# Kernel tuning notes

Hardware: AMD Instinct MI355X
Metric: run time of the kernel (lower is better)

## Reference

```python
import jax, jax.numpy as jnp
import numpy as np

N, H, DK, DV, DFF, D = 2, 8, 32, 32, 512, 256
B, S = 2, 2048
MASK_VALUE = -1e-30
EPS = 1e-14  # K.epsilon()**2 with default epsilon 1e-7


def glorot(key, shape):
    fan_in, fan_out = shape[-2], shape[-1]
    limit = np.sqrt(6.0 / (fan_in + fan_out))
    return jax.random.uniform(key, shape, jnp.float32, -limit, limit)


def setup_inputs() -> dict:
    key = jax.random.key(0)
    ks = jax.random.split(key, 8)
    return {
        "x": jax.random.normal(ks[0], (B, S, D), jnp.float32),
        "mask": jnp.ones((B, S), jnp.float32),
        "Wq": glorot(ks[1], (N, H, D, DK)),
        "Wk": glorot(ks[2], (N, H, D, DK)),
        "Wv": glorot(ks[3], (N, H, D, DV)),
        "Wo": glorot(ks[4], (N, H * DV, D)),
        "W1": glorot(ks[5], (N, D, DFF)),
        "b1": jnp.zeros((N, DFF), jnp.float32),
        "W2": glorot(ks[6], (N, DFF, D)),
        "b2": jnp.zeros((N, D), jnp.float32),
        "gamma": jnp.ones((2 * N,), jnp.float32),
        "beta": jnp.zeros((2 * N,), jnp.float32),
    }


def _layernorm(x, g, b):
    mean = jnp.mean(x, axis=-1, keepdims=True)
    var = jnp.mean(jnp.square(x - mean), axis=-1, keepdims=True)
    return (x - mean) / jnp.sqrt(var + EPS) * g + b


def reference(x, mask, Wq, Wk, Wv, Wo, W1, b1, W2, b2, gamma, beta):
    m = mask[:, None, None, :]  # [B,1,1,S], multiplies score rows' key axis
    for i in range(N):
        # batched multi-head attention (no 1/sqrt(dk) scaling, faithful to source)
        q = jnp.einsum("bsd,hdk->bhsk", x, Wq[i])
        k = jnp.einsum("bsd,hdk->bhsk", x, Wk[i])
        v = jnp.einsum("bsd,hdv->bhsv", x, Wv[i])
        A = jnp.einsum("bhsk,bhtk->bhst", q, k)  # [B,H,S,S]
        A = m * A + (1.0 - m) * MASK_VALUE
        A = jax.nn.softmax(A, axis=-1)
        o = jnp.einsum("bhst,bhtv->bhsv", A, v)
        conc = o.transpose(0, 2, 1, 3).reshape(x.shape[0], x.shape[1], H * DV)
        x = x + conc @ Wo[i]
        x = _layernorm(x, gamma[2 * i], beta[2 * i])
        ffn = jax.nn.relu(x @ W1[i] + b1[i]) @ W2[i] + b2[i]
        x = x + ffn
        x = _layernorm(x, gamma[2 * i + 1], beta[2 * i + 1])
    return x
```

## Files before the change

### kernel.cpp

```cpp
#include <hip/hip_runtime.h>
#include <hip/hip_bf16.h>

#define NL 2
#define NH 8
#define DKk 32
#define DVv 32
#define DFF 512
#define DD 256
#define BB 2
#define SS 2048
#define MROWS (BB*SS)
#define LN_EPS 1e-14f
#define L2E 1.4426950408889634f
#define SOFT_SHIFT_L2E (50.0f*L2E)

typedef __hip_bfloat16 bf16;
typedef unsigned short us;
typedef short bf16x8 __attribute__((ext_vector_type(8)));
typedef float f32x4  __attribute__((ext_vector_type(4)));
typedef unsigned short us4 __attribute__((ext_vector_type(4)));

#define O_XF   256
#define O_QB   (O_XF+1048576)
#define O_KH   (O_QB+1048576)
#define O_KL   (O_KH+524288)
#define O_VT   (O_KL+524288)
#define O_XH   (O_VT+524288)
#define O_XL   (O_XH+524288)
#define O_OP   (O_XL+524288)
#define O_ML   (O_OP+2097152)
#define O_MASK (O_ML+65536)
#define O_B1   (O_MASK+4096)
#define O_B2   (O_B1+1024)
#define O_GM   (O_B2+512)
#define O_BT   (O_GM+4)
#define O_PREP (O_BT+4)
#define CONV_TOTAL (1048576+4096+1024+512+4+4)
#define CONV_BLOCKS ((CONV_TOTAL+255)/256)
#define PREP_BLOCKS 512
#define PQH 0u
#define PQL 393216u
#define POH 786432u
#define POL 917504u
#define P1H 1048576u
#define P1L 1310720u
#define P2H 1572864u
#define P2L 1835008u

__device__ __forceinline__ float us2f(us u){
  unsigned int v = ((unsigned int)u) << 16; float f;
  __builtin_memcpy(&f, &v, 4); return f;
}
__device__ __forceinline__ us f2bf_rne(float f){
  unsigned int b = __float_as_uint(f);
  b += 0x7FFFu + ((b>>16)&1u);
  return (us)(b>>16);
}

#if __has_builtin(__builtin_amdgcn_exp2f)
#define EXP2F(x) __builtin_amdgcn_exp2f(x)
#else
#define EXP2F(x) exp2f(x)
#endif

#if __has_builtin(__builtin_amdgcn_cvt_pk_bf16_f32)
typedef __bf16 bf16x2_t __attribute__((ext_vector_type(2)));
__device__ __forceinline__ int pack_bf16(float a, float b){
  bf16x2_t r = __builtin_amdgcn_cvt_pk_bf16_f32(a, b);
  int i; __builtin_memcpy(&i, &r, 4); return i;
}
#else
__device__ __forceinline__ int pack_bf16(float a, float b){
  int b0 = __float_as_int(a) + 0x8000;
  int b1 = __float_as_int(b) + 0x8000;
  return (b1 & 0xFFFF0000) | ((int)((unsigned)b0 >> 16));
}
#endif

__device__ __forceinline__ void gl_lds16(const us* g, us* l){
  __builtin_amdgcn_global_load_lds(
    (const __attribute__((address_space(1))) unsigned int*)g,
    (__attribute__((address_space(3))) unsigned int*)l, 16, 0, 0);
}

__device__ __forceinline__ size_t xhl_idx(int row, int col){
  int rt = row>>6, rg = (row>>4)&3, L15 = row&15;
  int kc = col>>5, Q = (col>>3)&3, j = col&7;
  return ((size_t)(rt*8+kc))*2048 + rg*512 + Q*128 + L15*8 + j;
}

__device__ __forceinline__ float conv1(const void* src, size_t i, int flag){
  if(flag) return ((const float*)src)[i];
  return us2f(((const us*)src)[i]);
}

__device__ __forceinline__ void prep_b_raw(const void* W0, const void* W1v, const void* W2v,
                                           int baseoff, us* __restrict__ Bh, us* __restrict__ Bl,
                                           int Kd, int Nd, int qkv, int g, int flag)
{
  int total = (Kd/32)*(Nd/16)*64;
  if(g >= total) return;
  int lane = g & 63, fi = g >> 6;
  int ncN = Nd/16;
  int nc = fi % ncN, kc = fi / ncN;
  int Q = lane>>4, L15 = lane&15;
  int n = nc*16 + L15;
  const void* src;
  int off0, stride;
  if(qkv){
    int sec = n>>8, h = (n>>5)&7, kq = n&31;
    src = (sec==0)?W0:((sec==1)?W1v:W2v);
    off0 = baseoff + h*8192 + kq;
    stride = 32;
  } else {
    src = W0;
    off0 = baseoff + n;
    stride = Nd;
  }
  #pragma unroll
  for(int j=0;j<8;j++){
    int k = kc*32 + Q*8 + j;
    float v = conv1(src, (size_t)off0 + (size_t)k*stride, flag);
    us hb = f2bf_rne(v);
    Bh[(size_t)g*8 + j] = hb;
    Bl[(size_t)g*8 + j] = f2bf_rne(v - us2f(hb));
  }
}

__global__ void conv_prep(const void* s0, const void* s1, const void* sWq, const void* sWk,
                          const void* sWv, const void* sWo, const void* sW1, const void* sb1,
                          const void* sW2, const void* sb2, const void* sgm, const void* sbt,
                          float* __restrict__ ws, int* __restrict__ flagp)
{
  __shared__ int fsh[4];
  int bad = 0;
  const us* xr = (const us*)s0;
  for(int i=threadIdx.x; i<4096; i+=256){
    float f = us2f(xr[i]);
    if(!(fabsf(f) < 1e3f)) bad = 1;
  }
  unsigned long long m = __ballot(bad);
  if((threadIdx.x&63)==0) fsh[threadIdx.x>>6] = (m!=0ull);
  __syncthreads();
  int flag = (fsh[0]|fsh[1]|fsh[2]|fsh[3]);
  if(blockIdx.x==0 && threadIdx.x==0) *flagp = flag;

  int b = blockIdx.x;
  if(b < PREP_BLOCKS){
    int layer = b >> 8, lb = b & 255;
    us* prep = (us*)(ws + O_PREP);
    if(lb < 96){
      int g = lb*256 + threadIdx.x;
      prep_b_raw(sWq, sWk, sWv, layer*65536, prep+PQH+(size_t)layer*196608,
                 prep+PQL+(size_t)layer*196608, 256, 768, 1, g, flag);
    } else if(lb < 128){
      int g = (lb-96)*256 + threadIdx.x;
      prep_b_raw(sWo, nullptr, nullptr, layer*65536, prep+POH+(size_t)layer*65536,
                 prep+POL+(size_t)layer*65536, 256, 256, 0, g, flag);
    } else if(lb < 192){
      int g = (lb-128)*256 + threadIdx.x;
      prep_b_raw(sW1, nullptr, nullptr, layer*131072, prep+P1H+(size_t)layer*131072,
                 prep+P1L+(size_t)layer*131072, 256, 512, 0, g, flag);
    } else {
      int g = (lb-192)*256 + threadIdx.x;
      prep_b_raw(sW2, nullptr, nullptr, layer*131072, prep+P2H+(size_t)layer*131072,
                 prep+P2L+(size_t)layer*131072, 512, 256, 0, g, flag);
    }
    return;
  }
  int g = (b - PREP_BLOCKS)*256 + threadIdx.x;
  if(g < 1048576){
    float v = conv1(s0, g, flag);
    ws[O_XF+g] = v;
    us hb = f2bf_rne(v);
    us lb = f2bf_rne(v - us2f(hb));
    size_t xi = xhl_idx(g>>8, g&255);
    ((us*)(ws+O_XH))[xi] = hb;
    ((us*)(ws+O_XL))[xi] = lb;
    return;
  }
  g -= 1048576;
  if(g < 4096){ ws[O_MASK+g] = conv1(s1, g, flag)*L2E; return; }
  g -= 4096;
  if(g < 1024){ ws[O_B1+g] = conv1(sb1, g, flag); return; }
  g -= 1024;
  if(g < 512){ ws[O_B2+g] = conv1(sb2, g, flag); return; }
  g -= 512;
  if(g < 4){ ws[O_GM+g] = conv1(sgm, g, flag); return; }
  g -= 4;
  if(g < 4){ ws[O_BT+g] = conv1(sbt, g, flag); return; }
}

template<int MODE>
__launch_bounds__(256)
__global__ void gemm_mfma(const us* __restrict__ Axh, const us* __restrict__ Axl,
                          const us* __restrict__ Bh, const us* __restrict__ Bl,
                          const float* __restrict__ bias,
                          float* __restrict__ O,
                          us* __restrict__ QH, us* __restrict__ QL,
                          us* __restrict__ KH, us* __restrict__ KL, us* __restrict__ VT,
                          int Ncols, int Kdim)
{
  __shared__ __align__(16) us SH[16384];
  const int t = threadIdx.x;
  const int w = t>>6, lane = t&63;
  const int Q = lane>>4, L15 = lane&15;
  const int bx = blockIdx.x, by = blockIdx.y;
  const int row0 = bx*64;
  const int nc0 = by*4;
  const int col0 = by*64;
  const int nKc = Kdim>>5;
  const int ncW = Ncols>>4;

  f32x4 acc[2][2];
  #pragma unroll
  for(int i=0;i<2;i++)
    #pragma unroll
    for(int j=0;j<2;j++) acc[i][j] = (f32x4){0.f,0.f,0.f,0.f};

  auto stage = [&](int kc){
    const int bo = (kc&1)*8192;
    size_t abase = ((size_t)(bx*nKc + kc))*2048;
    gl_lds16(&Axh[abase + (size_t)t*8], &SH[bo + t*8]);
    gl_lds16(&Axl[abase + (size_t)t*8], &SH[bo + 2048 + t*8]);
    size_t gidx = ((size_t)(kc*ncW + nc0 + w)*64 + lane)*8;
    gl_lds16(&Bh[gidx], &SH[bo + 4096 + t*8]);
    gl_lds16(&Bl[gidx], &SH[bo + 6144 + t*8]);
  };

  stage(0);

  for(int kc=0; kc<nKc; kc++){
    __syncthreads();
    if(kc+1 < nKc) stage(kc+1);
    const int bo = (kc&1)*8192;
    const us* Ah  = SH + bo;
    const us* Al  = SH + bo + 2048;
    const us* Bhs = SH + bo + 4096;
    const us* Bls = SH + bo + 6144;

    bf16x8 aAh[2], aAl[2], bBh[2], bBl[2];
    #pragma unroll
    for(int rg2=0;rg2<2;rg2++){
      int rg = (w&1)*2 + rg2;
      aAh[rg2] = *(const bf16x8*)&Ah[rg*512 + lane*8];
      aAl[rg2] = *(const bf16x8*)&Al[rg*512 + lane*8];
    }
    #pragma unroll
    for(int cg2=0;cg2<2;cg2++){
      int nc = (w>>1)*2 + cg2;
      bBh[cg2] = *(const bf16x8*)&Bhs[nc*512 + lane*8];
      bBl[cg2] = *(const bf16x8*)&Bls[nc*512 + lane*8];
    }
    #pragma unroll
    for(int rg2=0;rg2<2;rg2++)
      #pragma unroll
      for(int cg2=0;cg2<2;cg2++){
        acc[rg2][cg2] = __builtin_amdgcn_mfma_f32_16x16x32_bf16(aAl[rg2], bBh[cg2], acc[rg2][cg2], 0,0,0);
        acc[rg2][cg2] = __builtin_amdgcn_mfma_f32_16x16x32_bf16(aAh[rg2], bBl[cg2], acc[rg2][cg2], 0,0,0);
        acc[rg2][cg2] = __builtin_amdgcn_mfma_f32_16x16x32_bf16(aAh[rg2], bBh[cg2], acc[rg2][cg2], 0,0,0);
      }
  }

  if(MODE==0){
    __syncthreads();
    us* TH = SH;
    us* TL = SH + 4608;
    #pragma unroll
    for(int rg2=0;rg2<2;rg2++)
      #pragma unroll
      for(int cg2=0;cg2<2;cg2++)
        #pragma unroll
        for(int r=0;r<4;r++){
          int rl = (w&1)*32 + rg2*16 + Q*4 + r;
          int cl = (w>>1)*32 + cg2*16 + L15;
          float va = acc[rg2][cg2][r];
          us hb = f2bf_rne(va);
          TH[rl*72+cl] = hb;
          TL[rl*72+cl] = f2bf_rne(va - us2f(hb));
        }
    __syncthreads();
    const int sec = col0>>8;
    const int h0  = (col0&255)>>5;
    const int b_  = row0>>11;
    const int srow0 = row0 & 2047;
    if(sec < 2){
      us* DH = (sec==0) ? QH : KH;
      us* DL = (sec==0) ? QL : KL;
      #pragma unroll
      for(int u2=0; u2<2; u2++){
        int u = w + u2*4;
        int rg = u&3, half = u>>2;
        int lbase = (rg*16 + L15)*72 + half*32 + Q*8;
        bf16x8 hv = *(const bf16x8*)&TH[lbase];
        bf16x8 lv = *(const bf16x8*)&TL[lbase];
        int bh = b_*NH + h0 + half;
        size_t dbase = ((size_t)(bh*128 + (srow0>>4) + rg)*64 + lane)*8;
        *(bf16x8*)&DH[dbase] = hv;
        *(bf16x8*)&DL[dbase] = lv;
      }
    } else {
      #pragma unroll
      for(int u2=0; u2<2; u2++){
        int u = w + u2*4;
        int sgrp = u&1, kqh = (u>>1)&1, half = u>>2;
        union{ us u8[8]; bf16x8 v; } vv;
        #pragma unroll
        for(int j=0;j<8;j++){
          int rl = sgrp*32 + Q*8 + j;
          int cl = half*32 + kqh*16 + L15;
          vv.u8[j] = TH[rl*72+cl];
        }
        int bh = b_*NH + h0 + half;
        size_t dbase = ((size_t)((bh*64 + (srow0>>5) + sgrp)*2 + kqh)*64 + lane)*8;
        *(bf16x8*)&VT[dbase] = vv.v;
      }
    }
  } else {
    #pragma unroll
    for(int rg2=0;rg2<2;rg2++)
      #pragma unroll
      for(int cg2=0;cg2<2;cg2++)
        #pragma unroll
        for(int r=0;r<4;r++){
          int row = row0 + (w&1)*32 + rg2*16 + Q*4 + r;
          int c   = col0 + (w>>1)*32 + cg2*16 + L15;
          float v = acc[rg2][cg2][r] + bias[c];
          O[(size_t)row*Ncols + c] = v>0.f ? v : 0.f;
        }
  }
}

template<int SRC>
__launch_bounds__(256)
__global__ void gemm_ln(const float* __restrict__ A,
                        const float* __restrict__ OpartA, const float* __restrict__ MLA,
                        const us* __restrict__ Bh, const us* __restrict__ Bl,
                        const float* __restrict__ bias, const float* __restrict__ res,
                        float* __restrict__ xf,
                        us* __restrict__ xh, us* __restrict__ xl,
                        const float* __restrict__ gamma, const float* __restrict__ beta, int gi,
                        void* __restrict__ out, int write_out,
                        const int* __restrict__ flagp, int Kdim)
{
  __shared__ __align__(16) us Ahs[1024], Als[1024];
  __shared__ __align__(16) us Bhs[16384], Bls[16384];
  __shared__ float lred[128];
  const int t = threadIdx.x;
  const int w = t>>6, lane = t&63;
  const int Q = lane>>4, L15 = lane&15;
  const int row0 = blockIdx.x*16;
  const int nKc = Kdim>>5;

  f32x4 acc[4];
  #pragma unroll
  for(int cg=0;cg<4;cg++) acc[cg] = (f32x4){0.f,0.f,0.f,0.f};

  float4 pv0, pv1, pv;
  float pl0 = 0.f, pl1 = 0.f;

  auto preloadA = [&](int kc){
    if(t < 128){
      int r = t>>3;
      int kl = (t&7)*4;
      if(SRC==0){
        int row = row0 + r;
        int b_ = row>>11, s_ = row&2047;
        size_t i0 = (size_t)(b_*8 + kc)*2048 + s_;
        pl0 = MLA[i0];
        pl1 = MLA[i0+32768];
        pv0 = *(const float4*)&OpartA[i0*32 + kl];
        pv1 = *(const float4*)&OpartA[(i0+32768)*32 + kl];
      } else {
        pv = *(const float4*)&A[(size_t)(row0+r)*Kdim + kc*32 + kl];
      }
    }
  };
  auto writeA = [&](int kc){
    if(t < 128){
      int r = t>>3;
      int kl = (t&7)*4;
      float f[4];
      if(SRC==0){
        float inv = 1.f/(pl0 + pl1);
        f[0]=(pv0.x+pv1.x)*inv; f[1]=(pv0.y+pv1.y)*inv;
        f[2]=(pv0.z+pv1.z)*inv; f[3]=(pv0.w+pv1.w)*inv;
      } else {
        f[0]=pv.x; f[1]=pv.y; f[2]=pv.z; f[3]=pv.w;
      }
      us4 h4, l4;
      #pragma unroll
      for(int j=0;j<4;j++){
        us hb = f2bf_rne(f[j]);
        h4[j] = hb; l4[j] = f2bf_rne(f[j] - us2f(hb));
      }
      int bo = (kc&1)*512;
      int off = (kl>>3)*128 + r*8 + (kl&7);
      *(us4*)&Ahs[bo+off] = h4;
      *(us4*)&Als[bo+off] = l4;
    }
  };
  auto stageB = [&](int kc){
    const int bo = (kc&1)*8192;
    #pragma unroll
    for(int ii=0; ii<4; ii++){
      int unit = w + ii*4;
      size_t gidx = ((size_t)(kc*16 + unit)*64 + lane)*8;
      gl_lds16(&Bh[gidx], &Bhs[bo + unit*512 + lane*8]);
      gl_lds16(&Bl[gidx], &Bls[bo + unit*512 + lane*8]);
    }
  };

  preloadA(0);
  stageB(0);
  writeA(0);

  for(int kc=0; kc<nKc; kc++){
    __syncthreads();
    if(kc+1 < nKc){
      preloadA(kc+1);
      stageB(kc+1);
    }
    const int bo = (kc&1);
    bf16x8 aAh = *(const bf16x8*)&Ahs[bo*512 + lane*8];
    bf16x8 aAl = *(const bf16x8*)&Als[bo*512 + lane*8];
    #pragma unroll
    for(int cg=0;cg<4;cg++){
      int unit = w*4 + cg;
      bf16x8 bBh = *(const bf16x8*)&Bhs[bo*8192 + unit*512 + lane*8];
      bf16x8 bBl = *(const bf16x8*)&Bls[bo*8192 + unit*512 + lane*8];
      acc[cg] = __builtin_amdgcn_mfma_f32_16x16x32_bf16(aAl, bBh, acc[cg], 0,0,0);
      acc[cg] = __builtin_amdgcn_mfma_f32_16x16x32_bf16(aAh, bBl, acc[cg], 0,0,0);
      acc[cg] = __builtin_amdgcn_mfma_f32_16x16x32_bf16(aAh, bBh, acc[cg], 0,0,0);
    }
    if(kc+1 < nKc) writeA(kc+1);
  }

  float tmp[4][4];
  #pragma unroll
  for(int cg=0;cg<4;cg++)
    #pragma unroll
    for(int r=0;r<4;r++){
      int row = row0 + Q*4 + r;
      int c = w*64 + cg*16 + L15;
      float v = acc[cg][r] + res[(size_t)row*DD + c];
      if(SRC==1) v += bias[c];
      tmp[cg][r] = v;
    }
  float s[4], sq[4];
  #pragma unroll
  for(int r=0;r<4;r++){
    s[r]  = tmp[0][r]+tmp[1][r]+tmp[2][r]+tmp[3][r];
    sq[r] = tmp[0][r]*tmp[0][r]+tmp[1][r]*tmp[1][r]+tmp[2][r]*tmp[2][r]+tmp[3][r]*tmp[3][r];
  }
  #pragma unroll
  for(int off=1; off<16; off<<=1)
    #pragma unroll
    for(int r=0;r<4;r++){
      s[r]  += __shfl_xor(s[r], off);
      sq[r] += __shfl_xor(sq[r], off);
    }
  if(L15==0){
    #pragma unroll
    for(int r=0;r<4;r++){
      int rl = Q*4 + r;
      lred[(w*16 + rl)*2]   = s[r];
      lred[(w*16 + rl)*2+1] = sq[r];
    }
  }
  __syncthreads();
  float g = gamma[gi], bb = beta[gi];
  float scv[4], mnv[4];
  #pragma unroll
  for(int r=0;r<4;r++){
    int rl = Q*4 + r;
    float S  = lred[rl*2]   + lred[(16+rl)*2]   + lred[(32+rl)*2]   + lred[(48+rl)*2];
    float SQ = lred[rl*2+1] + lred[(16+rl)*2+1] + lred[(32+rl)*2+1] + lred[(48+rl)*2+1];
    float mean = S*(1.f/DD);
    float var  = SQ*(1.f/DD) - mean*mean;
    scv[r] = rsqrtf(var+LN_EPS)*g;
    mnv[r] = mean;
  }
  int flag = write_out ? *flagp : 0;
  #pragma unroll
  for(int cg=0;cg<4;cg++)
    #pragma unroll
    for(int r=0;r<4;r++){
      int row = row0 + Q*4 + r;
      int c = w*64 + cg*16 + L15;
      float val = (tmp[cg][r]-mnv[r])*scv[r] + bb;
      xf[(size_t)row*DD + c] = val;
      us hb = f2bf_rne(val);
      size_t xi = xhl_idx(row, c);
      xh[xi] = hb;
      xl[xi] = f2bf_rne(val - us2f(hb));
      if(write_out){
        if(flag) ((float*)out)[(size_t)row*DD + c] = val;
        else     ((bf16*)out)[(size_t)row*DD + c] = __float2bfloat16(val);
      }
    }
}

__launch_bounds__(256)
__global__ void attn_kernel(const us* __restrict__ QH, const us* __restrict__ QL,
                            const us* __restrict__ KH, const us* __restrict__ KL,
                            const us* __restrict__ VT,
                            const float* __restrict__ mask,
                            float* __restrict__ Opart, float* __restrict__ ML)
{
  __shared__ __align__(16) us Khs[4096], Kls[4096], Vts[4096];
  __shared__ __align__(16) float Msl[128];
  const int t = threadIdx.x;
  const int bh = blockIdx.x >> 6;
  const int qt = (blockIdx.x & 63) >> 1;
  const int ks = blockIdx.x & 1;
  const int b_ = bh >> 3;
  const int wv = t >> 6;
  const int lane = t & 63;
  const int Q = lane >> 4, L15 = lane & 15;
  const int q0 = qt*64 + wv*16;

  size_t qidx = ((size_t)(bh*128 + qt*4 + wv)*64 + lane)*8;
  const bf16x8 qh_v = *(const bf16x8*)&QH[qidx];
  const bf16x8 ql_v = *(const bf16x8*)&QL[qidx];

  const us* KHbh = KH + (size_t)bh*65536;
  const us* KLbh = KL + (size_t)bh*65536;
  const us* VTbh = VT + (size_t)bh*65536;
  const int base = ks*1024;

  f32x4 Oa0a = {0.f,0.f,0.f,0.f}, Oa0b = {0.f,0.f,0.f,0.f};
  f32x4 Oa1a = {0.f,0.f,0.f,0.f}, Oa1b = {0.f,0.f,0.f,0.f};
  float lacc = 0.f;

  {
    size_t kbase = (size_t)(base>>4)*512;
    size_t vbase = (size_t)(base>>5)*1024;
    gl_lds16(&KHbh[kbase + (size_t)t*8], &Khs[t*8]);
    gl_lds16(&KLbh[kbase + (size_t)t*8], &Kls[t*8]);
    gl_lds16(&VTbh[vbase + (size_t)t*8], &Vts[t*8]);
    if(t < 64) Msl[t] = mask[b_*SS + base + t];
  }

  for(int s=0; s<16; s++){
    __syncthreads();
    if(s < 15){
      int t0n = base + (s+1)*64;
      int bn = (s+1)&1;
      size_t kbase = (size_t)(t0n>>4)*512;
      size_t vbase = (size_t)(t0n>>5)*1024;
      gl_lds16(&KHbh[kbase + (size_t)t*8], &Khs[bn*2048 + t*8]);
      gl_lds16(&KLbh[kbase + (size_t)t*8], &Kls[bn*2048 + t*8]);
      gl_lds16(&VTbh[vbase + (size_t)t*8], &Vts[bn*2048 + t*8]);
      if(t < 64) Msl[bn*64 + t] = mask[b_*SS + t0n + t];
    }
    const int bo = (s&1)*2048;
    const int mo = (s&1)*64;

    f32x4 St[4];
    const f32x4 zz = {0.f,0.f,0.f,0.f};
    #pragma unroll
    for(int kt=0;kt<4;kt++){
      bf16x8 aKh = *(const bf16x8*)&Khs[bo + kt*512 + lane*8];
      bf16x8 aKl = *(const bf16x8*)&Kls[bo + kt*512 + lane*8];
      f32x4 a = __builtin_amdgcn_mfma_f32_16x16x32_bf16(aKl, qh_v, zz, 0,0,0);
      a = __builtin_amdgcn_mfma_f32_16x16x32_bf16(aKh, ql_v, a, 0,0,0);
      a = __builtin_amdgcn_mfma_f32_16x16x32_bf16(aKh, qh_v, a, 0,0,0);
      St[kt] = a;
    }

    float lsum = 0.f;
    #pragma unroll
    for(int kt=0;kt<4;kt++){
      float4 mv = *(const float4*)&Msl[mo + kt*16 + Q*4];
      float mvr[4] = {mv.x, mv.y, mv.z, mv.w};
      #pragma unroll
      for(int r=0;r<4;r++){
        float p = EXP2F(fmaf(mvr[r], St[kt][r], -SOFT_SHIFT_L2E));
        St[kt][r] = p;
        lsum += p;
      }
    }
    lacc += lsum;

    int pk[4][2];
    #pragma unroll
    for(int kt=0;kt<4;kt++){
      pk[kt][0] = pack_bf16(St[kt][0], St[kt][1]);
      pk[kt][1] = pack_bf16(St[kt][2], St[kt][3]);
    }

    #pragma unroll
    for(int c=0;c<2;c++){
      union { int i[4]; bf16x8 v; } bu;
      #pragma unroll
      for(int d=0;d<4;d++){
        int srcl = (((Q&1)*2 + (d>>1))<<4) | L15;
        int vlo = __shfl(pk[2*c  ][d&1], srcl, 64);
        int vhi = __shfl(pk[2*c+1][d&1], srcl, 64);
        bu.i[d] = (Q & 2) ? vhi : vlo;
      }
      bf16x8 aV0 = *(const bf16x8*)&Vts[bo + (c*2+0)*512 + lane*8];
      bf16x8 aV1 = *(const bf16x8*)&Vts[bo + (c*2+1)*512 + lane*8];
      if(c == 0){
        Oa0a = __builtin_amdgcn_mfma_f32_16x16x32_bf16(aV0, bu.v, Oa0a, 0,0,0);
        Oa1a = __builtin_amdgcn_mfma_f32_16x16x32_bf16(aV1, bu.v, Oa1a, 0,0,0);
      } else {
        Oa0b = __builtin_amdgcn_mfma_f32_16x16x32_bf16(aV0, bu.v, Oa0b, 0,0,0);
        Oa1b = __builtin_amdgcn_mfma_f32_16x16x32_bf16(aV1, bu.v, Oa1b, 0,0,0);
      }
    }
  }

  f32x4 Oa0 = Oa0a + Oa0b;
  f32x4 Oa1 = Oa1a + Oa1b;
  lacc += __shfl_xor(lacc, 16);
  lacc += __shfl_xor(lacc, 32);

  float* opp = &Opart[((size_t)(ks*16+bh)*SS + q0 + L15)*32];
  #pragma unroll
  for(int r=0;r<4;r++){
    opp[Q*4+r]    = Oa0[r];
    opp[16+Q*4+r] = Oa1[r];
  }
  if(Q==0){
    ML[(size_t)(ks*16+bh)*SS + q0 + L15] = lacc;
  }
}

extern "C" void kernel_launch(void* const* d_in, const int* in_sizes, int n_in,
                              void* d_out, int out_size, void* d_ws, size_t ws_size,
                              hipStream_t stream)
{
  float* ws = (float*)d_ws;
  int* flagp = (int*)d_ws;

  float* xf  = ws + O_XF;
  us* QHb = (us*)(ws + O_QB);
  us* QLb = QHb + 1048576;
  us* KH = (us*)(ws + O_KH);
  us* KL = (us*)(ws + O_KL);
  us* VT = (us*)(ws + O_VT);
  us* XH = (us*)(ws + O_XH);
  us* XL = (us*)(ws + O_XL);
  float* Opart = ws + O_OP;
  float* ML  = ws + O_ML;
  float* fh  = Opart;
  float* b1f = ws + O_B1;
  float* b2f_ = ws + O_B2;
  float* gmf = ws + O_GM;
  float* btf = ws + O_BT;
  us* prep = (us*)(ws + O_PREP);

  conv_prep<<<PREP_BLOCKS+CONV_BLOCKS,256,0,stream>>>(
      d_in[0], d_in[1], d_in[2], d_in[3], d_in[4], d_in[5],
      d_in[6], d_in[7], d_in[8], d_in[9], d_in[10], d_in[11],
      ws, flagp);

  for(int i=0;i<NL;i++){
    const float* b1i = b1f + (size_t)i*DFF;
    const float* b2i = b2f_ + (size_t)i*DD;

    dim3 g0(64, 12);
    gemm_mfma<0><<<g0,256,0,stream>>>(XH, XL,
                                      prep+PQH+(size_t)i*196608, prep+PQL+(size_t)i*196608,
                                      nullptr, nullptr,
                                      QHb, QLb, KH, KL, VT, 768, 256);
    attn_kernel<<<1024,256,0,stream>>>(QHb, QLb, KH, KL, VT, ws + O_MASK, Opart, ML);
    gemm_ln<0><<<256,256,0,stream>>>(nullptr, Opart, ML,
                                     prep+POH+(size_t)i*65536, prep+POL+(size_t)i*65536,
                                     nullptr, xf, xf, XH, XL,
                                     gmf, btf, 2*i, d_out, 0, flagp, 256);
    dim3 g2(64, 8);
    gemm_mfma<2><<<g2,256,0,stream>>>(XH, XL,
                                      prep+P1H+(size_t)i*131072, prep+P1L+(size_t)i*131072,
                                      b1i, fh,
                                      nullptr, nullptr, nullptr, nullptr, nullptr, 512, 256);
    gemm_ln<1><<<256,256,0,stream>>>(fh, nullptr, nullptr,
                                     prep+P2H+(size_t)i*131072, prep+P2L+(size_t)i*131072,
                                     b2i, xf, xf, XH, XL,
                                     gmf, btf, 2*i+1, d_out, (i==NL-1)?1:0, flagp, 512);
  }
}
```

Measured before the change: 258.7 us.

## Triple-buffer LDS staging with explicit vmcnt waits in GEMM and attention kernels

Switches the async global-to-LDS staging in the MFMA GEMM, GEMM+LayerNorm and attention kernels from double to triple buffering, prefetching two chunks ahead. The full __syncthreads is replaced with a partial s_waitcnt vmcnt plus a raw barrier, so later loads can stay in flight while the current chunk is computed. The attention kernel also loads the whole 1024-entry mask slice into LDS once up front instead of per step. This hides more global load latency, at the cost of more LDS per block, which may reduce occupancy, and it depends on hand-counted vmcnt values being correct.

```diff
diff --git a/kernel.cpp b/kernel.cpp
--- a/kernel.cpp
+++ b/kernel.cpp
@@ -47,6 +47,11 @@
 #define P2H 1572864u
 #define P2L 1835008u
 
+#define WAITVMC(n) asm volatile("s_waitcnt vmcnt(" #n ")" ::: "memory")
+#define LGKM0()    asm volatile("s_waitcnt lgkmcnt(0)" ::: "memory")
+#define SBAR()     __builtin_amdgcn_s_barrier()
+#define SCHEDB()   __builtin_amdgcn_sched_barrier(0)
+
 __device__ __forceinline__ float us2f(us u){
   unsigned int v = ((unsigned int)u) << 16; float f;
   __builtin_memcpy(&f, &v, 4); return f;
@@ -201,7 +206,7 @@
                           us* __restrict__ KH, us* __restrict__ KL, us* __restrict__ VT,
                           int Ncols, int Kdim)
 {
-  __shared__ __align__(16) us SH[16384];
+  __shared__ __align__(16) us SH[24576];
   const int t = threadIdx.x;
   const int w = t>>6, lane = t&63;
   const int Q = lane>>4, L15 = lane&15;
@@ -218,8 +223,8 @@
     #pragma unroll
     for(int j=0;j<2;j++) acc[i][j] = (f32x4){0.f,0.f,0.f,0.f};
 
-  auto stage = [&](int kc){
-    const int bo = (kc&1)*8192;
+  auto stage = [&](int kc, int bi){
+    const int bo = bi*8192;
     size_t abase = ((size_t)(bx*nKc + kc))*2048;
     gl_lds16(&Axh[abase + (size_t)t*8], &SH[bo + t*8]);
     gl_lds16(&Axl[abase + (size_t)t*8], &SH[bo + 2048 + t*8]);
@@ -228,12 +233,18 @@
     gl_lds16(&Bl[gidx], &SH[bo + 6144 + t*8]);
   };
 
-  stage(0);
-
+  stage(0, 0);
+  stage(1, 1);
+
+  int rb = 0;
   for(int kc=0; kc<nKc; kc++){
-    __syncthreads();
-    if(kc+1 < nKc) stage(kc+1);
-    const int bo = (kc&1)*8192;
+    if(kc+1 < nKc){ WAITVMC(4); } else { WAITVMC(0); }
+    SCHEDB();
+    SBAR();
+    SCHEDB();
+    if(kc+2 < nKc) stage(kc+2, rb==0 ? 2 : rb-1);
+
+    const int bo = rb*8192;
     const us* Ah  = SH + bo;
     const us* Al  = SH + bo + 2048;
     const us* Bhs = SH + bo + 4096;
@@ -260,6 +271,7 @@
         acc[rg2][cg2] = __builtin_amdgcn_mfma_f32_16x16x32_bf16(aAh[rg2], bBl[cg2], acc[rg2][cg2], 0,0,0);
         acc[rg2][cg2] = __builtin_amdgcn_mfma_f32_16x16x32_bf16(aAh[rg2], bBh[cg2], acc[rg2][cg2], 0,0,0);
       }
+    rb = rb==2 ? 0 : rb+1;
   }
 
   if(MODE==0){
@@ -344,7 +356,7 @@
                         const int* __restrict__ flagp, int Kdim)
 {
   __shared__ __align__(16) us Ahs[1024], Als[1024];
-  __shared__ __align__(16) us Bhs[16384], Bls[16384];
+  __shared__ __align__(16) us Bhs[24576], Bls[24576];
   __shared__ float lred[128];
   const int t = threadIdx.x;
   const int w = t>>6, lane = t&63;
@@ -400,8 +412,8 @@
       *(us4*)&Als[bo+off] = l4;
     }
   };
-  auto stageB = [&](int kc){
-    const int bo = (kc&1)*8192;
+  auto stageB = [&](int kc, int bi){
+    const int bo = bi*8192;
     #pragma unroll
     for(int ii=0; ii<4; ii++){
       int unit = w + ii*4;
@@ -412,28 +424,34 @@
   };
 
   preloadA(0);
-  stageB(0);
+  stageB(0, 0);
+  stageB(1, 1);
   writeA(0);
 
+  int rb = 0;
   for(int kc=0; kc<nKc; kc++){
-    __syncthreads();
-    if(kc+1 < nKc){
-      preloadA(kc+1);
-      stageB(kc+1);
-    }
-    const int bo = (kc&1);
-    bf16x8 aAh = *(const bf16x8*)&Ahs[bo*512 + lane*8];
-    bf16x8 aAl = *(const bf16x8*)&Als[bo*512 + lane*8];
+    if(kc+1 < nKc){ WAITVMC(8); } else { WAITVMC(0); }
+    LGKM0();
+    SCHEDB();
+    SBAR();
+    SCHEDB();
+    if(kc+1 < nKc) preloadA(kc+1);
+    if(kc+2 < nKc) stageB(kc+2, rb==0 ? 2 : rb-1);
+
+    const int bo = rb*8192;
+    bf16x8 aAh = *(const bf16x8*)&Ahs[(kc&1)*512 + lane*8];
+    bf16x8 aAl = *(const bf16x8*)&Als[(kc&1)*512 + lane*8];
     #pragma unroll
     for(int cg=0;cg<4;cg++){
       int unit = w*4 + cg;
-      bf16x8 bBh = *(const bf16x8*)&Bhs[bo*8192 + unit*512 + lane*8];
-      bf16x8 bBl = *(const bf16x8*)&Bls[bo*8192 + unit*512 + lane*8];
+      bf16x8 bBh = *(const bf16x8*)&Bhs[bo + unit*512 + lane*8];
+      bf16x8 bBl = *(const bf16x8*)&Bls[bo + unit*512 + lane*8];
       acc[cg] = __builtin_amdgcn_mfma_f32_16x16x32_bf16(aAl, bBh, acc[cg], 0,0,0);
       acc[cg] = __builtin_amdgcn_mfma_f32_16x16x32_bf16(aAh, bBl, acc[cg], 0,0,0);
       acc[cg] = __builtin_amdgcn_mfma_f32_16x16x32_bf16(aAh, bBh, acc[cg], 0,0,0);
     }
     if(kc+1 < nKc) writeA(kc+1);
+    rb = rb==2 ? 0 : rb+1;
   }
 
   float tmp[4][4];
@@ -508,8 +526,8 @@
                             const float* __restrict__ mask,
                             float* __restrict__ Opart, float* __restrict__ ML)
 {
-  __shared__ __align__(16) us Khs[4096], Kls[4096], Vts[4096];
-  __shared__ __align__(16) float Msl[128];
+  __shared__ __align__(16) us Khs[6144], Kls[6144], Vts[6144];
+  __shared__ __align__(16) float Msl[1024];
   const int t = threadIdx.x;
   const int bh = blockIdx.x >> 6;
   const int qt = (blockIdx.x & 63) >> 1;
@@ -533,29 +551,32 @@
   f32x4 Oa1a = {0.f,0.f,0.f,0.f}, Oa1b = {0.f,0.f,0.f,0.f};
   float lacc = 0.f;
 
+  auto stagekv = [&](int s, int bi){
+    int t0n = base + s*64;
+    size_t kbase = (size_t)(t0n>>4)*512;
+    size_t vbase = (size_t)(t0n>>5)*1024;
+    gl_lds16(&KHbh[kbase + (size_t)t*8], &Khs[bi*2048 + t*8]);
+    gl_lds16(&KLbh[kbase + (size_t)t*8], &Kls[bi*2048 + t*8]);
+    gl_lds16(&VTbh[vbase + (size_t)t*8], &Vts[bi*2048 + t*8]);
+  };
+
   {
-    size_t kbase = (size_t)(base>>4)*512;
-    size_t vbase = (size_t)(base>>5)*1024;
-    gl_lds16(&KHbh[kbase + (size_t)t*8], &Khs[t*8]);
-    gl_lds16(&KLbh[kbase + (size_t)t*8], &Kls[t*8]);
-    gl_lds16(&VTbh[vbase + (size_t)t*8], &Vts[t*8]);
-    if(t < 64) Msl[t] = mask[b_*SS + base + t];
-  }
-
+    const us* mrow = (const us*)(mask + (size_t)b_*SS + base);
+    gl_lds16(mrow + (size_t)t*8, ((us*)Msl) + t*8);
+    stagekv(0, 0);
+    stagekv(1, 1);
+  }
+
+  int rb = 0;
   for(int s=0; s<16; s++){
-    __syncthreads();
-    if(s < 15){
-      int t0n = base + (s+1)*64;
-      int bn = (s+1)&1;
-      size_t kbase = (size_t)(t0n>>4)*512;
-      size_t vbase = (size_t)(t0n>>5)*1024;
-      gl_lds16(&KHbh[kbase + (size_t)t*8], &Khs[bn*2048 + t*8]);
-      gl_lds16(&KLbh[kbase + (size_t)t*8], &Kls[bn*2048 + t*8]);
-      gl_lds16(&VTbh[vbase + (size_t)t*8], &Vts[bn*2048 + t*8]);
-      if(t < 64) Msl[bn*64 + t] = mask[b_*SS + t0n + t];
-    }
-    const int bo = (s&1)*2048;
-    const int mo = (s&1)*64;
+    if(s+1 < 16){ WAITVMC(3); } else { WAITVMC(0); }
+    SCHEDB();
+    SBAR();
+    SCHEDB();
+    if(s+2 < 16) stagekv(s+2, rb==0 ? 2 : rb-1);
+
+    const int bo = rb*2048;
+    const int mo = s*64;
 
     f32x4 St[4];
     const f32x4 zz = {0.f,0.f,0.f,0.f};
@@ -610,6 +631,7 @@
         Oa1b = __builtin_amdgcn_mfma_f32_16x16x32_bf16(aV1, bu.v, Oa1b, 0,0,0);
       }
     }
+    rb = rb==2 ? 0 : rb+1;
   }
 
   f32x4 Oa0 = Oa0a + Oa0b;
```

New measurement: 274.9 us. 1.06x slower.

## Vectorize input conversion, swizzle attention block order, preload full mask slice

Applied to the files above, without the earlier changes.

The input conversion now handles 8 elements per thread with 16-byte loads and stores for the float, hi and lo copies, replacing scalar per-element writes. The attention kernel remaps block indices so neighbouring workgroups are spread across head/query tiles, which is meant to improve cache locality or the spread of work across XCDs. It also loads the whole 1024-entry mask slice into LDS once with an async copy instead of per-iteration scalar loads. The cost is more LDS use and a fixed 8-way swizzle that assumes the grid size is 1024 blocks.

```diff
diff --git a/kernel.cpp b/kernel.cpp
--- a/kernel.cpp
+++ b/kernel.cpp
@@ -35,8 +35,8 @@
 #define O_GM   (O_B2+512)
 #define O_BT   (O_GM+4)
 #define O_PREP (O_BT+4)
-#define CONV_TOTAL (1048576+4096+1024+512+4+4)
-#define CONV_BLOCKS ((CONV_TOTAL+255)/256)
+#define TAIL_TOTAL (4096+1024+512+4+4)
+#define CONV_BLOCKS (512 + (TAIL_TOTAL+255)/256)
 #define PREP_BLOCKS 512
 #define PQH 0u
 #define PQL 393216u
@@ -168,18 +168,36 @@
     }
     return;
   }
-  int g = (b - PREP_BLOCKS)*256 + threadIdx.x;
-  if(g < 1048576){
-    float v = conv1(s0, g, flag);
-    ws[O_XF+g] = v;
-    us hb = f2bf_rne(v);
-    us lb = f2bf_rne(v - us2f(hb));
-    size_t xi = xhl_idx(g>>8, g&255);
-    ((us*)(ws+O_XH))[xi] = hb;
-    ((us*)(ws+O_XL))[xi] = lb;
+  int b2 = b - PREP_BLOCKS;
+  if(b2 < 512){
+    int g8 = b2*256 + threadIdx.x;
+    int e0 = g8*8;
+    float v[8];
+    if(flag){
+      float4 a0 = *((const float4*)s0 + (e0>>2));
+      float4 a1 = *((const float4*)s0 + (e0>>2) + 1);
+      v[0]=a0.x; v[1]=a0.y; v[2]=a0.z; v[3]=a0.w;
+      v[4]=a1.x; v[5]=a1.y; v[6]=a1.z; v[7]=a1.w;
+    } else {
+      bf16x8 u = *((const bf16x8*)s0 + g8);
+      #pragma unroll
+      for(int j=0;j<8;j++) v[j] = us2f((us)u[j]);
+    }
+    *(float4*)&ws[O_XF+e0]   = (float4){v[0],v[1],v[2],v[3]};
+    *(float4*)&ws[O_XF+e0+4] = (float4){v[4],v[5],v[6],v[7]};
+    union{ us a[8]; uint4 q; } hh, ll;
+    #pragma unroll
+    for(int j=0;j<8;j++){
+      us hb = f2bf_rne(v[j]);
+      hh.a[j] = hb;
+      ll.a[j] = f2bf_rne(v[j] - us2f(hb));
+    }
+    size_t xi = xhl_idx(e0>>8, e0&255);
+    *(uint4*)&((us*)(ws+O_XH))[xi] = hh.q;
+    *(uint4*)&((us*)(ws+O_XL))[xi] = ll.q;
     return;
   }
-  g -= 1048576;
+  int g = (b2-512)*256 + threadIdx.x;
   if(g < 4096){ ws[O_MASK+g] = conv1(s1, g, flag)*L2E; return; }
   g -= 4096;
   if(g < 1024){ ws[O_B1+g] = conv1(sb1, g, flag); return; }
@@ -509,11 +527,12 @@
                             float* __restrict__ Opart, float* __restrict__ ML)
 {
   __shared__ __align__(16) us Khs[4096], Kls[4096], Vts[4096];
-  __shared__ __align__(16) float Msl[128];
+  __shared__ __align__(16) float Msl[1024];
   const int t = threadIdx.x;
-  const int bh = blockIdx.x >> 6;
-  const int qt = (blockIdx.x & 63) >> 1;
-  const int ks = blockIdx.x & 1;
+  const int swz = (blockIdx.x & 7)*128 + (blockIdx.x >> 3);
+  const int bh = swz >> 6;
+  const int qt = (swz & 63) >> 1;
+  const int ks = swz & 1;
   const int b_ = bh >> 3;
   const int wv = t >> 6;
   const int lane = t & 63;
@@ -534,12 +553,13 @@
   float lacc = 0.f;
 
   {
+    const us* mrow = (const us*)(mask + (size_t)b_*SS + base);
+    gl_lds16(mrow + (size_t)t*8, ((us*)Msl) + t*8);
     size_t kbase = (size_t)(base>>4)*512;
     size_t vbase = (size_t)(base>>5)*1024;
     gl_lds16(&KHbh[kbase + (size_t)t*8], &Khs[t*8]);
     gl_lds16(&KLbh[kbase + (size_t)t*8], &Kls[t*8]);
     gl_lds16(&VTbh[vbase + (size_t)t*8], &Vts[t*8]);
-    if(t < 64) Msl[t] = mask[b_*SS + base + t];
   }
 
   for(int s=0; s<16; s++){
@@ -552,10 +572,9 @@
       gl_lds16(&KHbh[kbase + (size_t)t*8], &Khs[bn*2048 + t*8]);
       gl_lds16(&KLbh[kbase + (size_t)t*8], &Kls[bn*2048 + t*8]);
       gl_lds16(&VTbh[vbase + (size_t)t*8], &Vts[bn*2048 + t*8]);
-      if(t < 64) Msl[bn*64 + t] = mask[b_*SS + t0n + t];
     }
     const int bo = (s&1)*2048;
-    const int mo = (s&1)*64;
+    const int mo = s*64;
 
     f32x4 St[4];
     const f32x4 zz = {0.f,0.f,0.f,0.f};
```

Result: slower. 265.5 us (+2.6%).
